# Kernel tuning notes

Measured on AMD Instinct MI355X. Metric: run time of the kernel, lower is better.

Reference implementation:

```python
import jax, jax.numpy as jnp
import numpy as np

N = 50000    # nodes
E = 800000   # edges
F = 128      # node_feature_dim
H = 128      # GCN hidden
H2 = 64      # fc1 hidden
T = 8        # num_tactics
G = 64       # graphs in batch


def setup_inputs() -> dict:
    key = jax.random.key(0)
    ks = jax.random.split(key, 12)
    s = 0.05
    return {
        "x": jax.random.normal(ks[0], (N, F), jnp.float32),
        "edge_index": jax.random.randint(ks[1], (2, E), 0, N, dtype=jnp.int32),
        "batch": jnp.sort(jax.random.randint(ks[2], (N,), 0, G, dtype=jnp.int32)),
        "W": jax.random.normal(ks[3], (F, H), jnp.float32) * s,
        "b": jax.random.normal(ks[4], (H,), jnp.float32) * s,
        "fc1_w": jax.random.normal(ks[5], (H, H2), jnp.float32) * s,
        "fc1_b": jax.random.normal(ks[6], (H2,), jnp.float32) * s,
        "actor_w": jax.random.normal(ks[7], (H2, T), jnp.float32) * s,
        "actor_b": jax.random.normal(ks[8], (T,), jnp.float32) * s,
        "critic_w": jax.random.normal(ks[9], (H2, 1), jnp.float32) * s,
        "critic_b": jax.random.normal(ks[10], (1,), jnp.float32) * s,
    }


def _gcn_conv(x, edge_index, W, b):
    # PyG GCNConv: add self-loops, symmetric D^-1/2 (A+I) D^-1/2 normalization,
    # linear transform first, then scatter-add aggregation, then bias.
    n = x.shape[0]
    loops = jnp.arange(n, dtype=edge_index.dtype)
    src = jnp.concatenate([edge_index[0], loops])  # message sources (x_j)
    dst = jnp.concatenate([edge_index[1], loops])  # aggregation targets
    deg = jax.ops.segment_sum(jnp.ones_like(dst, jnp.float32), dst, num_segments=N)
    dinv = deg ** -0.5  # deg >= 1 due to self-loops
    norm = dinv[src] * dinv[dst]                   # [E+N]
    h = x @ W                                      # [N, H]
    msgs = h[src] * norm[:, None]                  # [E+N, H]
    return jax.ops.segment_sum(msgs, dst, num_segments=N) + b


def reference(x, edge_index, batch, W, b, fc1_w, fc1_b, actor_w, actor_b, critic_w, critic_b):
    h = jax.nn.relu(_gcn_conv(x, edge_index, W, b))            # [N, H]
    # global_mean_pool over batch index
    sums = jax.ops.segment_sum(h, batch, num_segments=G)       # [G, H]
    cnts = jax.ops.segment_sum(jnp.ones((h.shape[0],), h.dtype), batch, num_segments=G)
    group_state = sums / jnp.maximum(cnts, 1.0)[:, None]
    z = jax.nn.relu(group_state @ fc1_w + fc1_b)               # [G, H2]
    tactic_probs = jax.nn.softmax(z @ actor_w + actor_b, axis=-1)  # [G, T]
    group_value = z @ critic_w + critic_b                      # [G, 1]
    return tactic_probs, group_value
```

## Files before the change

kernel.cpp:

```cpp
#include <hip/hip_runtime.h>
#include <hip/hip_bf16.h>

#define NN 50000
#define EE 800000
#define FF 128
#define HH 128
#define HID2 64
#define TT 8
#define GG 64
#define NB 196
#define NSB 256
#define EPB (EE / NSB)

__device__ inline unsigned short f2bf(float f) {
    union { float f; unsigned u; } v; v.f = f;
    unsigned r = v.u + 0x7fff + ((v.u >> 16) & 1);
    return (unsigned short)(r >> 16);
}

__global__ __launch_bounds__(256) void kb1(const int* __restrict__ dst,
                                           int* __restrict__ table) {
    __shared__ int cnt[NB];
    int t = threadIdx.x, blk = blockIdx.x;
    for (int i = t; i < NB; i += 256) cnt[i] = 0;
    __syncthreads();
    int e0 = blk * EPB;
    for (int e = e0 + t; e < e0 + EPB; e += 256)
        atomicAdd(&cnt[dst[e] >> 8], 1);
    __syncthreads();
    for (int i = t; i < NB; i += 256) table[blk * NB + i] = cnt[i];
}

__global__ __launch_bounds__(256) void kb2(int* __restrict__ table,
                                           int* __restrict__ bbase) {
    __shared__ int s[256];
    int b = threadIdx.x;
    int tot = 0;
    if (b < NB)
        for (int blk = 0; blk < NSB; blk++) tot += table[blk * NB + b];
    s[b] = (b < NB) ? tot : 0;
    __syncthreads();
    for (int off = 1; off < 256; off <<= 1) {
        int a = s[b];
        int w = (b >= off) ? s[b - off] : 0;
        __syncthreads();
        s[b] = a + w;
        __syncthreads();
    }
    int base = (b == 0) ? 0 : s[b - 1];
    if (b < NB) {
        bbase[b] = base;
        int run = base;
        for (int blk = 0; blk < NSB; blk++) {
            int v = table[blk * NB + b];
            table[blk * NB + b] = run;
            run += v;
        }
    }
    if (b == 0) bbase[NB] = EE;
}

__global__ __launch_bounds__(256) void kb3(const int* __restrict__ src,
                                           const int* __restrict__ dst,
                                           const int* __restrict__ table,
                                           unsigned* __restrict__ etmp) {
    __shared__ int ofs[NB];
    __shared__ int cur[NB];
    int t = threadIdx.x, blk = blockIdx.x;
    for (int i = t; i < NB; i += 256) { ofs[i] = table[blk * NB + i]; cur[i] = 0; }
    __syncthreads();
    int e0 = blk * EPB;
    for (int e = e0 + t; e < e0 + EPB; e += 256) {
        int d = dst[e];
        int b = d >> 8;
        int r = atomicAdd(&cur[b], 1);
        etmp[ofs[b] + r] = ((unsigned)d << 16) | (unsigned)src[e];
    }
}

__global__ __launch_bounds__(256) void k_csr(const unsigned* __restrict__ etmp,
                                             const int* __restrict__ bbase,
                                             int* __restrict__ row_ptr,
                                             float* __restrict__ dinv,
                                             int* __restrict__ srcs) {
    __shared__ int s[256];
    __shared__ int cur[256];
    int t = threadIdx.x, b = blockIdx.x;
    s[t] = 0;
    __syncthreads();
    int e0 = bbase[b], e1 = bbase[b + 1];
    for (int e = e0 + t; e < e1; e += 256)
        atomicAdd(&s[(etmp[e] >> 16) & 255], 1);
    __syncthreads();
    int v = s[t];
    for (int off = 1; off < 256; off <<= 1) {
        int a = s[t];
        int w = (t >= off) ? s[t - off] : 0;
        __syncthreads();
        s[t] = a + w;
        __syncthreads();
    }
    int excl = s[t] - v + e0;
    int node = b * 256 + t;
    if (node < NN) {
        row_ptr[node] = excl;
        dinv[node] = rsqrtf((float)(v + 1));
    }
    if (b == NB - 1 && t == 0) row_ptr[NN] = EE;
    cur[t] = excl;
    __syncthreads();
    for (int e = e0 + t; e < e1; e += 256) {
        unsigned u = etmp[e];
        int slot = atomicAdd(&cur[(u >> 16) & 255], 1);
        srcs[slot] = (int)(u & 0xffffu);
    }
}

__global__ __launch_bounds__(256) void k_gemm(const float* __restrict__ x,
                                              const float* __restrict__ W,
                                              const float* __restrict__ dinv,
                                              unsigned* __restrict__ hs) {
    __shared__ float xs[64 * 36];
    __shared__ float ws[32 * 132];
    int tid = threadIdx.x;
    int tx = tid & 15, ty = tid >> 4;
    int r0 = blockIdx.x * 64;
    float acc[4][8];
#pragma unroll
    for (int r = 0; r < 4; r++)
#pragma unroll
        for (int c = 0; c < 8; c++) acc[r][c] = 0.f;

    for (int k0 = 0; k0 < 128; k0 += 32) {
        {
            int row = tid >> 2, q = tid & 3;
            int gr = r0 + row;
            float4 a0 = {0, 0, 0, 0}, a1 = {0, 0, 0, 0};
            if (gr < NN) {
                const float4* p = (const float4*)(x + (size_t)gr * 128 + k0 + q * 8);
                a0 = p[0]; a1 = p[1];
            }
            float* dp = &xs[row * 36 + q * 8];
            ((float4*)dp)[0] = a0; ((float4*)dp)[1] = a1;
        }
        {
            int kr = tid >> 3, q = tid & 7;
            const float4* p = (const float4*)(W + (size_t)(k0 + kr) * 128 + q * 16);
            float4 b0 = p[0], b1 = p[1], b2 = p[2], b3 = p[3];
            float* dp = &ws[kr * 132 + q * 16];
            ((float4*)dp)[0] = b0; ((float4*)dp)[1] = b1;
            ((float4*)dp)[2] = b2; ((float4*)dp)[3] = b3;
        }
        __syncthreads();
#pragma unroll
        for (int kk = 0; kk < 32; kk++) {
            float a[4];
#pragma unroll
            for (int r = 0; r < 4; r++) a[r] = xs[(ty * 4 + r) * 36 + kk];
            float4 b0 = *(const float4*)&ws[kk * 132 + tx * 8];
            float4 b1 = *(const float4*)&ws[kk * 132 + tx * 8 + 4];
            float bv[8] = {b0.x, b0.y, b0.z, b0.w, b1.x, b1.y, b1.z, b1.w};
#pragma unroll
            for (int r = 0; r < 4; r++)
#pragma unroll
                for (int c = 0; c < 8; c++)
                    acc[r][c] = fmaf(a[r], bv[c], acc[r][c]);
        }
        __syncthreads();
    }
#pragma unroll
    for (int r = 0; r < 4; r++) {
        int gr = r0 + ty * 4 + r;
        if (gr < NN) {
            float di = dinv[gr];
            unsigned p0 = f2bf(acc[r][0] * di) | ((unsigned)f2bf(acc[r][1] * di) << 16);
            unsigned p1 = f2bf(acc[r][2] * di) | ((unsigned)f2bf(acc[r][3] * di) << 16);
            unsigned p2 = f2bf(acc[r][4] * di) | ((unsigned)f2bf(acc[r][5] * di) << 16);
            unsigned p3 = f2bf(acc[r][6] * di) | ((unsigned)f2bf(acc[r][7] * di) << 16);
            uint4 o = {p0, p1, p2, p3};
            *(uint4*)(hs + (size_t)gr * 64 + tx * 4) = o;
        }
    }
}

__global__ __launch_bounds__(256) void k_aggr(const uint4* __restrict__ hs4,
                                              const int* __restrict__ row_ptr,
                                              const int* __restrict__ srcs,
                                              const float* __restrict__ dinv,
                                              const float* __restrict__ bias,
                                              const int* __restrict__ batch,
                                              float* __restrict__ gsum) {
    __shared__ float gacc[8 * 128];
    int tid = threadIdx.x;
    int qid = tid >> 4, sub = tid & 15;
    int i_base = blockIdx.x * 32;
    int g_first = batch[i_base];
    int last = i_base + 31; if (last >= NN) last = NN - 1;
    int gspan = batch[last] - g_first + 1;
    bool lds_pool = (gspan <= 8);
    int slots = lds_pool ? gspan : 0;
    for (int idx = tid; idx < slots * 128; idx += 256) gacc[idx] = 0.f;
    __syncthreads();

    const float4* b4 = (const float4*)(bias + sub * 8);
    float4 bb0 = b4[0], bb1 = b4[1];

    float racc[8];
#pragma unroll
    for (int j = 0; j < 8; j++) racc[j] = 0.f;
    int cur_lg = -1;

    for (int n = 0; n < 2; n++) {
        int i = i_base + qid * 2 + n;
        if (i >= NN) break;
        int lg = batch[i] - g_first;
        if (lg != cur_lg) {
            if (cur_lg >= 0) {
                float* gp = lds_pool ? &gacc[cur_lg * 128 + sub * 8]
                                     : &gsum[(g_first + cur_lg) * 128 + sub * 8];
#pragma unroll
                for (int j = 0; j < 8; j++) atomicAdd(&gp[j], racc[j]);
#pragma unroll
                for (int j = 0; j < 8; j++) racc[j] = 0.f;
            }
            cur_lg = lg;
        }
        float di = dinv[i];
        uint4 su = hs4[(size_t)i * 16 + sub];
        float a0 = __uint_as_float(su.x << 16);
        float a1 = __uint_as_float(su.x & 0xffff0000u);
        float a2 = __uint_as_float(su.y << 16);
        float a3 = __uint_as_float(su.y & 0xffff0000u);
        float a4 = __uint_as_float(su.z << 16);
        float a5 = __uint_as_float(su.z & 0xffff0000u);
        float a6 = __uint_as_float(su.w << 16);
        float a7 = __uint_as_float(su.w & 0xffff0000u);
        int e = row_ptr[i], e1 = row_ptr[i + 1];
        for (; e + 3 < e1; e += 4) {
            int s0 = srcs[e], s1 = srcs[e + 1], s2 = srcs[e + 2], s3 = srcs[e + 3];
            uint4 u0 = hs4[(size_t)s0 * 16 + sub];
            uint4 u1 = hs4[(size_t)s1 * 16 + sub];
            uint4 u2 = hs4[(size_t)s2 * 16 + sub];
            uint4 u3 = hs4[(size_t)s3 * 16 + sub];
            a0 += __uint_as_float(u0.x << 16); a1 += __uint_as_float(u0.x & 0xffff0000u);
            a2 += __uint_as_float(u0.y << 16); a3 += __uint_as_float(u0.y & 0xffff0000u);
            a4 += __uint_as_float(u0.z << 16); a5 += __uint_as_float(u0.z & 0xffff0000u);
            a6 += __uint_as_float(u0.w << 16); a7 += __uint_as_float(u0.w & 0xffff0000u);
            a0 += __uint_as_float(u1.x << 16); a1 += __uint_as_float(u1.x & 0xffff0000u);
            a2 += __uint_as_float(u1.y << 16); a3 += __uint_as_float(u1.y & 0xffff0000u);
            a4 += __uint_as_float(u1.z << 16); a5 += __uint_as_float(u1.z & 0xffff0000u);
            a6 += __uint_as_float(u1.w << 16); a7 += __uint_as_float(u1.w & 0xffff0000u);
            a0 += __uint_as_float(u2.x << 16); a1 += __uint_as_float(u2.x & 0xffff0000u);
            a2 += __uint_as_float(u2.y << 16); a3 += __uint_as_float(u2.y & 0xffff0000u);
            a4 += __uint_as_float(u2.z << 16); a5 += __uint_as_float(u2.z & 0xffff0000u);
            a6 += __uint_as_float(u2.w << 16); a7 += __uint_as_float(u2.w & 0xffff0000u);
            a0 += __uint_as_float(u3.x << 16); a1 += __uint_as_float(u3.x & 0xffff0000u);
            a2 += __uint_as_float(u3.y << 16); a3 += __uint_as_float(u3.y & 0xffff0000u);
            a4 += __uint_as_float(u3.z << 16); a5 += __uint_as_float(u3.z & 0xffff0000u);
            a6 += __uint_as_float(u3.w << 16); a7 += __uint_as_float(u3.w & 0xffff0000u);
        }
        for (; e < e1; ++e) {
            uint4 u0 = hs4[(size_t)srcs[e] * 16 + sub];
            a0 += __uint_as_float(u0.x << 16); a1 += __uint_as_float(u0.x & 0xffff0000u);
            a2 += __uint_as_float(u0.y << 16); a3 += __uint_as_float(u0.y & 0xffff0000u);
            a4 += __uint_as_float(u0.z << 16); a5 += __uint_as_float(u0.z & 0xffff0000u);
            a6 += __uint_as_float(u0.w << 16); a7 += __uint_as_float(u0.w & 0xffff0000u);
        }
        racc[0] += fmaxf(fmaf(a0, di, bb0.x), 0.f);
        racc[1] += fmaxf(fmaf(a1, di, bb0.y), 0.f);
        racc[2] += fmaxf(fmaf(a2, di, bb0.z), 0.f);
        racc[3] += fmaxf(fmaf(a3, di, bb0.w), 0.f);
        racc[4] += fmaxf(fmaf(a4, di, bb1.x), 0.f);
        racc[5] += fmaxf(fmaf(a5, di, bb1.y), 0.f);
        racc[6] += fmaxf(fmaf(a6, di, bb1.z), 0.f);
        racc[7] += fmaxf(fmaf(a7, di, bb1.w), 0.f);
    }
    if (cur_lg >= 0) {
        float* gp = lds_pool ? &gacc[cur_lg * 128 + sub * 8]
                             : &gsum[(g_first + cur_lg) * 128 + sub * 8];
#pragma unroll
        for (int j = 0; j < 8; j++) atomicAdd(&gp[j], racc[j]);
    }
    __syncthreads();
    for (int idx = tid; idx < slots * 128; idx += 256) {
        float v = gacc[idx];
        if (v != 0.f)
            atomicAdd(&gsum[(g_first + (idx >> 7)) * 128 + (idx & 127)], v);
    }
}

__device__ inline int lbound(const int* __restrict__ a, int n, int key) {
    int lo = 0, hi = n;
    while (lo < hi) {
        int mid = (lo + hi) >> 1;
        if (a[mid] < key) lo = mid + 1;
        else hi = mid;
    }
    return lo;
}

__global__ __launch_bounds__(64) void k_head(const float* __restrict__ gsum,
                                             const int* __restrict__ batch,
                                             const float* __restrict__ fc1_w,
                                             const float* __restrict__ fc1_b,
                                             const float* __restrict__ actor_w,
                                             const float* __restrict__ actor_b,
                                             const float* __restrict__ critic_w,
                                             const float* __restrict__ critic_b,
                                             float* __restrict__ out) {
    __shared__ float gs[128];
    __shared__ float zs[64];
    __shared__ float ls[8], es[8];
    int g = blockIdx.x, t = threadIdx.x;
    int lo = lbound(batch, NN, g), hi = lbound(batch, NN, g + 1);
    float invc = 1.f / fmaxf((float)(hi - lo), 1.f);
    gs[t] = gsum[g * 128 + t] * invc;
    gs[t + 64] = gsum[g * 128 + 64 + t] * invc;
    __syncthreads();
    float z = fc1_b[t];
    for (int k = 0; k < 128; k++) z = fmaf(gs[k], fc1_w[k * 64 + t], z);
    zs[t] = fmaxf(z, 0.f);
    __syncthreads();
    if (t < 8) {
        float l = actor_b[t];
        for (int k = 0; k < 64; k++) l = fmaf(zs[k], actor_w[k * 8 + t], l);
        ls[t] = l;
    }
    __syncthreads();
    if (t < 8) {
        float m = ls[0];
#pragma unroll
        for (int j = 1; j < 8; j++) m = fmaxf(m, ls[j]);
        es[t] = expf(ls[t] - m);
    }
    __syncthreads();
    if (t < 8) {
        float ssum = 0.f;
#pragma unroll
        for (int j = 0; j < 8; j++) ssum += es[j];
        out[g * 8 + t] = es[t] / ssum;
    }
    if (t == 32) {
        float v = critic_b[0];
        for (int k = 0; k < 64; k++) v = fmaf(zs[k], critic_w[k], v);
        out[GG * TT + g] = v;
    }
}

extern "C" void kernel_launch(void* const* d_in, const int* in_sizes, int n_in,
                              void* d_out, int out_size, void* d_ws, size_t ws_size,
                              hipStream_t stream) {
    const float* x        = (const float*)d_in[0];
    const int*   ei       = (const int*)d_in[1];
    const int*   batch    = (const int*)d_in[2];
    const float* W        = (const float*)d_in[3];
    const float* b        = (const float*)d_in[4];
    const float* fc1_w    = (const float*)d_in[5];
    const float* fc1_b    = (const float*)d_in[6];
    const float* actor_w  = (const float*)d_in[7];
    const float* actor_b  = (const float*)d_in[8];
    const float* critic_w = (const float*)d_in[9];
    const float* critic_b = (const float*)d_in[10];
    float* out = (float*)d_out;

    char* ws = (char*)d_ws;
    size_t off = 0;
    unsigned* hs     = (unsigned*)(ws + off); off += (size_t)NN * 64 * 4;
    float* dinv      = (float*)(ws + off);    off += (size_t)NN * 4;
    int*   row_ptr   = (int*)(ws + off);      off += (size_t)(NN + 1) * 4 + 12;
    int*   srcs      = (int*)(ws + off);      off += (size_t)EE * 4;
    unsigned* etmp   = (unsigned*)(ws + off); off += (size_t)EE * 4;
    int*   table     = (int*)(ws + off);      off += (size_t)NSB * NB * 4;
    int*   bbase     = (int*)(ws + off);      off += (size_t)(NB + 1) * 4;
    float* gsum      = (float*)(ws + off);    off += (size_t)GG * HH * 4;

    hipMemsetAsync(gsum, 0, (size_t)GG * HH * 4, stream);

    const int* src = ei;
    const int* dst = ei + EE;

    kb1<<<NSB, 256, 0, stream>>>(dst, table);
    kb2<<<1, 256, 0, stream>>>(table, bbase);
    kb3<<<NSB, 256, 0, stream>>>(src, dst, table, etmp);
    k_csr<<<NB, 256, 0, stream>>>(etmp, bbase, row_ptr, dinv, srcs);
    k_gemm<<<(NN + 63) / 64, 256, 0, stream>>>(x, W, dinv, hs);
    k_aggr<<<(NN + 31) / 32, 256, 0, stream>>>((const uint4*)hs, row_ptr, srcs,
                                               dinv, b, batch, gsum);
    k_head<<<GG, 64, 0, stream>>>(gsum, batch, fc1_w, fc1_b, actor_w, actor_b,
                                  critic_w, critic_b, out);
}
```

Measured before the change: 216.4 us.

## Use bf16 MFMA for node transform and parallelize bucket offset scan

Converts x and the transposed W to bf16 in separate pre-pass kernels, then replaces the FP32 shared-memory tiled GEMM with MFMA 16x16x32 bf16 instructions that read fragments directly from global memory. Separately, the single-block serial bucket prefix scan is split into a per-bucket parallel scan over 196 blocks plus a small scan of bucket totals. The aim is to cut GEMM compute time and the serial scan latency. The cost is two extra passes over the inputs, bf16 rounding of x and W, and scattered 2-byte stores of the output.

```diff
diff --git a/kernel.cpp b/kernel.cpp
--- a/kernel.cpp
+++ b/kernel.cpp
@@ -11,11 +11,39 @@
 #define NB 196
 #define NSB 256
 #define EPB (EE / NSB)
+#define NPAD 50048
+
+using frag_ab = __attribute__((ext_vector_type(8))) short;
+using frag_cd = __attribute__((ext_vector_type(4))) float;
 
 __device__ inline unsigned short f2bf(float f) {
     union { float f; unsigned u; } v; v.f = f;
     unsigned r = v.u + 0x7fff + ((v.u >> 16) & 1);
     return (unsigned short)(r >> 16);
+}
+
+__global__ __launch_bounds__(256) void kconv(const float* __restrict__ x,
+                                             unsigned short* __restrict__ x_bf) {
+    size_t gid = (size_t)blockIdx.x * 256 + threadIdx.x;
+    size_t i8 = gid * 8;
+    unsigned short o[8];
+    if (i8 < (size_t)NN * 128) {
+        const float4* p = (const float4*)(x + i8);
+        float4 a = p[0], b = p[1];
+        o[0] = f2bf(a.x); o[1] = f2bf(a.y); o[2] = f2bf(a.z); o[3] = f2bf(a.w);
+        o[4] = f2bf(b.x); o[5] = f2bf(b.y); o[6] = f2bf(b.z); o[7] = f2bf(b.w);
+    } else {
+#pragma unroll
+        for (int j = 0; j < 8; j++) o[j] = 0;
+    }
+    *(uint4*)(x_bf + i8) = *(const uint4*)o;
+}
+
+__global__ __launch_bounds__(256) void kwt(const float* __restrict__ W,
+                                           unsigned short* __restrict__ wt_bf) {
+    int gid = blockIdx.x * 256 + threadIdx.x;
+    int c = gid >> 7, k = gid & 127;
+    wt_bf[gid] = f2bf(W[k * 128 + c]);
 }
 
 __global__ __launch_bounds__(256) void kb1(const int* __restrict__ dst,
@@ -31,14 +59,30 @@
     for (int i = t; i < NB; i += 256) table[blk * NB + i] = cnt[i];
 }
 
-__global__ __launch_bounds__(256) void kb2(int* __restrict__ table,
-                                           int* __restrict__ bbase) {
+__global__ __launch_bounds__(256) void kb2a(int* __restrict__ table,
+                                            int* __restrict__ ctot) {
+    __shared__ int s[256];
+    int t = threadIdx.x, b = blockIdx.x;
+    int v = table[t * NB + b];
+    s[t] = v;
+    __syncthreads();
+    for (int off = 1; off < 256; off <<= 1) {
+        int a = s[t];
+        int w = (t >= off) ? s[t - off] : 0;
+        __syncthreads();
+        s[t] = a + w;
+        __syncthreads();
+    }
+    table[t * NB + b] = s[t] - v;
+    if (t == 255) ctot[b] = s[255];
+}
+
+__global__ __launch_bounds__(256) void kb2b(const int* __restrict__ ctot,
+                                            int* __restrict__ bbase) {
     __shared__ int s[256];
     int b = threadIdx.x;
-    int tot = 0;
-    if (b < NB)
-        for (int blk = 0; blk < NSB; blk++) tot += table[blk * NB + b];
-    s[b] = (b < NB) ? tot : 0;
+    int v = (b < NB) ? ctot[b] : 0;
+    s[b] = v;
     __syncthreads();
     for (int off = 1; off < 256; off <<= 1) {
         int a = s[b];
@@ -47,27 +91,22 @@
         s[b] = a + w;
         __syncthreads();
     }
-    int base = (b == 0) ? 0 : s[b - 1];
-    if (b < NB) {
-        bbase[b] = base;
-        int run = base;
-        for (int blk = 0; blk < NSB; blk++) {
-            int v = table[blk * NB + b];
-            table[blk * NB + b] = run;
-            run += v;
-        }
-    }
+    if (b < NB) bbase[b] = s[b] - v;
     if (b == 0) bbase[NB] = EE;
 }
 
 __global__ __launch_bounds__(256) void kb3(const int* __restrict__ src,
                                            const int* __restrict__ dst,
                                            const int* __restrict__ table,
+                                           const int* __restrict__ bbase,
                                            unsigned* __restrict__ etmp) {
     __shared__ int ofs[NB];
     __shared__ int cur[NB];
     int t = threadIdx.x, blk = blockIdx.x;
-    for (int i = t; i < NB; i += 256) { ofs[i] = table[blk * NB + i]; cur[i] = 0; }
+    for (int i = t; i < NB; i += 256) {
+        ofs[i] = table[blk * NB + i] + bbase[i];
+        cur[i] = 0;
+    }
     __syncthreads();
     int e0 = blk * EPB;
     for (int e = e0 + t; e < e0 + EPB; e += 256) {
@@ -116,69 +155,35 @@
     }
 }
 
-__global__ __launch_bounds__(256) void k_gemm(const float* __restrict__ x,
-                                              const float* __restrict__ W,
+__global__ __launch_bounds__(256) void k_gemm(const unsigned short* __restrict__ x_bf,
+                                              const unsigned short* __restrict__ wt_bf,
                                               const float* __restrict__ dinv,
-                                              unsigned* __restrict__ hs) {
-    __shared__ float xs[64 * 36];
-    __shared__ float ws[32 * 132];
+                                              unsigned short* __restrict__ hs) {
     int tid = threadIdx.x;
-    int tx = tid & 15, ty = tid >> 4;
-    int r0 = blockIdx.x * 64;
-    float acc[4][8];
-#pragma unroll
-    for (int r = 0; r < 4; r++)
-#pragma unroll
-        for (int c = 0; c < 8; c++) acc[r][c] = 0.f;
-
+    int w = tid >> 6, lane = tid & 63;
+    int m = lane & 15, quad = lane >> 4;
+    int r0 = blockIdx.x * 64 + w * 16;
+    frag_cd acc[8];
+#pragma unroll
+    for (int nt = 0; nt < 8; nt++) acc[nt] = frag_cd{0.f, 0.f, 0.f, 0.f};
+
+#pragma unroll
     for (int k0 = 0; k0 < 128; k0 += 32) {
-        {
-            int row = tid >> 2, q = tid & 3;
-            int gr = r0 + row;
-            float4 a0 = {0, 0, 0, 0}, a1 = {0, 0, 0, 0};
-            if (gr < NN) {
-                const float4* p = (const float4*)(x + (size_t)gr * 128 + k0 + q * 8);
-                a0 = p[0]; a1 = p[1];
-            }
-            float* dp = &xs[row * 36 + q * 8];
-            ((float4*)dp)[0] = a0; ((float4*)dp)[1] = a1;
+        frag_ab a = *(const frag_ab*)(x_bf + (size_t)(r0 + m) * 128 + k0 + quad * 8);
+#pragma unroll
+        for (int nt = 0; nt < 8; nt++) {
+            frag_ab bfr = *(const frag_ab*)(wt_bf + (size_t)(nt * 16 + m) * 128 + k0 + quad * 8);
+            acc[nt] = __builtin_amdgcn_mfma_f32_16x16x32_bf16(a, bfr, acc[nt], 0, 0, 0);
         }
-        {
-            int kr = tid >> 3, q = tid & 7;
-            const float4* p = (const float4*)(W + (size_t)(k0 + kr) * 128 + q * 16);
-            float4 b0 = p[0], b1 = p[1], b2 = p[2], b3 = p[3];
-            float* dp = &ws[kr * 132 + q * 16];
-            ((float4*)dp)[0] = b0; ((float4*)dp)[1] = b1;
-            ((float4*)dp)[2] = b2; ((float4*)dp)[3] = b3;
-        }
-        __syncthreads();
-#pragma unroll
-        for (int kk = 0; kk < 32; kk++) {
-            float a[4];
-#pragma unroll
-            for (int r = 0; r < 4; r++) a[r] = xs[(ty * 4 + r) * 36 + kk];
-            float4 b0 = *(const float4*)&ws[kk * 132 + tx * 8];
-            float4 b1 = *(const float4*)&ws[kk * 132 + tx * 8 + 4];
-            float bv[8] = {b0.x, b0.y, b0.z, b0.w, b1.x, b1.y, b1.z, b1.w};
-#pragma unroll
-            for (int r = 0; r < 4; r++)
-#pragma unroll
-                for (int c = 0; c < 8; c++)
-                    acc[r][c] = fmaf(a[r], bv[c], acc[r][c]);
-        }
-        __syncthreads();
-    }
-#pragma unroll
-    for (int r = 0; r < 4; r++) {
-        int gr = r0 + ty * 4 + r;
+    }
+#pragma unroll
+    for (int reg = 0; reg < 4; reg++) {
+        int gr = r0 + quad * 4 + reg;
         if (gr < NN) {
             float di = dinv[gr];
-            unsigned p0 = f2bf(acc[r][0] * di) | ((unsigned)f2bf(acc[r][1] * di) << 16);
-            unsigned p1 = f2bf(acc[r][2] * di) | ((unsigned)f2bf(acc[r][3] * di) << 16);
-            unsigned p2 = f2bf(acc[r][4] * di) | ((unsigned)f2bf(acc[r][5] * di) << 16);
-            unsigned p3 = f2bf(acc[r][6] * di) | ((unsigned)f2bf(acc[r][7] * di) << 16);
-            uint4 o = {p0, p1, p2, p3};
-            *(uint4*)(hs + (size_t)gr * 64 + tx * 4) = o;
+#pragma unroll
+            for (int nt = 0; nt < 8; nt++)
+                hs[(size_t)gr * 128 + nt * 16 + m] = f2bf(acc[nt][reg] * di);
         }
     }
 }
@@ -365,13 +370,16 @@
 
     char* ws = (char*)d_ws;
     size_t off = 0;
-    unsigned* hs     = (unsigned*)(ws + off); off += (size_t)NN * 64 * 4;
+    unsigned short* hs    = (unsigned short*)(ws + off); off += (size_t)NN * 128 * 2 + 64;
+    unsigned short* x_bf  = (unsigned short*)(ws + off); off += (size_t)NPAD * 128 * 2;
+    unsigned short* wt_bf = (unsigned short*)(ws + off); off += (size_t)128 * 128 * 2;
     float* dinv      = (float*)(ws + off);    off += (size_t)NN * 4;
     int*   row_ptr   = (int*)(ws + off);      off += (size_t)(NN + 1) * 4 + 12;
     int*   srcs      = (int*)(ws + off);      off += (size_t)EE * 4;
     unsigned* etmp   = (unsigned*)(ws + off); off += (size_t)EE * 4;
     int*   table     = (int*)(ws + off);      off += (size_t)NSB * NB * 4;
-    int*   bbase     = (int*)(ws + off);      off += (size_t)(NB + 1) * 4;
+    int*   bbase     = (int*)(ws + off);      off += (size_t)(NB + 1) * 4 + 12;
+    int*   ctot      = (int*)(ws + off);      off += (size_t)NB * 4 + 16;
     float* gsum      = (float*)(ws + off);    off += (size_t)GG * HH * 4;
 
     hipMemsetAsync(gsum, 0, (size_t)GG * HH * 4, stream);
@@ -379,11 +387,14 @@
     const int* src = ei;
     const int* dst = ei + EE;
 
+    kconv<<<(NPAD * 128 / 8 + 255) / 256, 256, 0, stream>>>(x, x_bf);
+    kwt<<<64, 256, 0, stream>>>(W, wt_bf);
     kb1<<<NSB, 256, 0, stream>>>(dst, table);
-    kb2<<<1, 256, 0, stream>>>(table, bbase);
-    kb3<<<NSB, 256, 0, stream>>>(src, dst, table, etmp);
+    kb2a<<<NB, 256, 0, stream>>>(table, ctot);
+    kb2b<<<1, 256, 0, stream>>>(ctot, bbase);
+    kb3<<<NSB, 256, 0, stream>>>(src, dst, table, bbase, etmp);
     k_csr<<<NB, 256, 0, stream>>>(etmp, bbase, row_ptr, dinv, srcs);
-    k_gemm<<<(NN + 63) / 64, 256, 0, stream>>>(x, W, dinv, hs);
+    k_gemm<<<NPAD / 64, 256, 0, stream>>>(x_bf, wt_bf, dinv, hs);
     k_aggr<<<(NN + 31) / 32, 256, 0, stream>>>((const uint4*)hs, row_ptr, srcs,
                                                dinv, b, batch, gsum);
     k_head<<<GG, 64, 0, stream>>>(gsum, batch, fc1_w, fc1_b, actor_w, actor_b,
```

Result: faster. 199.1 us (-8.0%).
